# Kernel tuning notes

Hardware: AMD Instinct MI355X
Metric: run time of the kernel (lower is better)

## Reference

```python
import jax, jax.numpy as jnp
import numpy as np

B, S, IN_DIM, HID, H, CS = 4, 4096, 1024, 1024, 16, 16
HD = HID // H
LN_EPS = 1e-5


def setup_inputs() -> dict:
    key = jax.random.key(0)
    ks = jax.random.split(key, 6)
    x = jax.random.normal(ks[0], (B, S, IN_DIM), jnp.float32)
    W_in = jax.random.normal(ks[1], (HID, IN_DIM), jnp.float32) * (IN_DIM ** -0.5)
    ln_g = jnp.ones((HID,), jnp.float32)
    ln_b = jnp.zeros((HID,), jnp.float32)
    W_gate = jax.random.normal(ks[2], (2 * H, HID), jnp.float32) * (HID ** -0.5)
    b_gate = jnp.zeros((2 * H,), jnp.float32)
    raw = 0.5 * float(np.log(1.9 / 0.1))  # atanh(0.9), as in _init_eigenvalues
    eig_raw = jnp.full((H,), raw, jnp.float32) + 0.01 * jax.random.normal(ks[3], (H,), jnp.float32)
    W_out = jax.random.normal(ks[4], (HID, HID), jnp.float32) * (HID ** -0.5)
    return {"x": x, "W_in": W_in, "ln_g": ln_g, "ln_b": ln_b,
            "W_gate": W_gate, "b_gate": b_gate, "eig_raw": eig_raw, "W_out": W_out}


def _chunk_scan(a, b):
    # a: (B,S,H) decay, b: (B,S,H,HD) input; h_t = a_t*h_{t-1} + b_t, h0 = 0
    Bsz, Sl = a.shape[0], a.shape[1]
    N = Sl // CS  # seq_len chosen divisible by chunk_size (pad_len == 0)
    ac = a.reshape(Bsz, N, CS, H)
    bc = b.reshape(Bsz, N, CS, H, HD)
    cum = jnp.cumprod(ac, axis=2)  # (B,N,C,H)
    ones = jnp.ones((Bsz, N, 1, H), a.dtype)
    cum_pad = jnp.concatenate([ones, cum[:, :, :-1]], axis=2)  # shifted cumprod
    # M[i,j] = cum_i / cum_pad_j for i>j, 1 on diag, 0 above
    Mi = cum[:, :, :, None, :]        # (B,N,C,1,H)
    Mj = cum_pad[:, :, None, :, :]    # (B,N,1,C,H)
    M = jnp.where(jnp.abs(Mj) > 1e-8, Mi / Mj, jnp.zeros_like(Mi))
    tril = jnp.tril(jnp.ones((CS, CS), a.dtype))[None, None, :, :, None]
    eye = jnp.eye(CS, dtype=a.dtype)[None, None, :, :, None]
    M = M * tril
    M = M * (1 - eye) + eye  # force exact 1 on diagonal
    # within-chunk contribution: (B,N,C,H,HD)
    h_contrib = jnp.einsum('bnijh,bnjhd->bnihd', M, bc)
    # inter-chunk sequential carry
    cum_T = jnp.moveaxis(cum, 1, 0)            # (N,B,C,H)
    hc_T = jnp.moveaxis(h_contrib, 1, 0)       # (N,B,C,H,HD)

    def step(h, inp):
        cum_n, hc_n = inp
        h_chunk = cum_n[..., None] * h[:, None] + hc_n  # (B,C,H,HD)
        return h_chunk[:, -1], h_chunk

    h0 = jnp.zeros((Bsz, H, HD), a.dtype)
    _, h_all = jax.lax.scan(step, h0, (cum_T, hc_T))   # (N,B,C,H,HD)
    h_all = jnp.moveaxis(h_all, 0, 1).reshape(Bsz, Sl, HID)
    return h_all


def reference(x, W_in, ln_g, ln_b, W_gate, b_gate, eig_raw, W_out):
    Bsz, Sl, _ = x.shape
    xp = x @ W_in.T                               # (B,S,HID)
    mu = jnp.mean(xp, axis=-1, keepdims=True)
    var = jnp.mean((xp - mu) ** 2, axis=-1, keepdims=True)
    xp = (xp - mu) * jax.lax.rsqrt(var + LN_EPS) * ln_g + ln_b
    gates = xp @ W_gate.T + b_gate                # (B,S,2H)
    alpha = jax.nn.sigmoid(gates[..., :H])
    beta = jax.nn.sigmoid(gates[..., H:])
    eig = jnp.tanh(eig_raw)                       # (H,)
    a = eig[None, None, :] * alpha                # (B,S,H)
    x_heads = xp.reshape(Bsz, Sl, H, HD)
    b = beta[..., None] * x_heads                 # (B,S,H,HD)
    h_all = _chunk_scan(a, b)                     # (B,S,HID)
    output = h_all @ W_out.T                      # dropout is identity in eval
    h_final = h_all[:, -1, :]
    return output, h_final
```

## Files before the change

### kernel.cpp

```cpp
#include <hip/hip_runtime.h>
#include <hip/hip_bf16.h>
#include <stdint.h>

#define BATCH 4
#define SEQ   4096
#define HID   1024
#define NH    16
#define HD    64
#define CS    16
#define NCH   256
#define MROWS 16384

typedef __attribute__((ext_vector_type(8))) __bf16 bf16x8;
typedef __attribute__((ext_vector_type(4))) float  f32x4;

__device__ __forceinline__ unsigned short f2bf(float f) {
    union { float f; unsigned u; } x; x.f = f;
    unsigned r = x.u + 0x7FFFu + ((x.u >> 16) & 1u);
    return (unsigned short)(r >> 16);
}
__device__ __forceinline__ float bf2f(unsigned short v) {
    union { unsigned u; float f; } x; x.u = ((unsigned)v) << 16;
    return x.f;
}

__device__ __forceinline__ void async_copy16(void* lds, const void* g) {
    __builtin_amdgcn_global_load_lds(
        (const __attribute__((address_space(1))) unsigned int*)g,
        (__attribute__((address_space(3))) unsigned int*)lds,
        16, 0, 0);
}

#define FENCE() asm volatile("" ::: "memory")
#define BARRIER() do { FENCE(); __builtin_amdgcn_s_barrier(); FENCE(); } while (0)

__global__ __launch_bounds__(256) void convert_all_kernel(
    const float* __restrict__ x, const float* __restrict__ W_in,
    const float* __restrict__ W_out, const float* __restrict__ W_gate,
    unsigned short* __restrict__ xb, unsigned short* __restrict__ Wib,
    unsigned short* __restrict__ Wob, unsigned short* __restrict__ Wgb)
{
    int i = blockIdx.x * 256 + threadIdx.x;
    const float4* src; ushort4* dst; int j;
    if (i < 4194304)      { src = (const float4*)x;      dst = (ushort4*)xb;  j = i; }
    else if (i < 4456448) { src = (const float4*)W_in;   dst = (ushort4*)Wib; j = i - 4194304; }
    else if (i < 4718592) { src = (const float4*)W_out;  dst = (ushort4*)Wob; j = i - 4456448; }
    else if (i < 4726784) { src = (const float4*)W_gate; dst = (ushort4*)Wgb; j = i - 4718592; }
    else return;
    float4 v = src[j];
    ushort4 o;
    o.x = f2bf(v.x); o.y = f2bf(v.y); o.z = f2bf(v.z); o.w = f2bf(v.w);
    dst[j] = o;
}

#define GBM 256
#define GBN 256
#define GBK 64

__global__ __launch_bounds__(512, 2) void gemm256_kernel(
    const unsigned short* __restrict__ A,
    const unsigned short* __restrict__ Bm,
    float* __restrict__ C, int M, int N, int K)
{
    __shared__ unsigned short As[2][GBM][GBK];
    __shared__ unsigned short Bs[2][GBN][GBK];

    const int t = threadIdx.x;
    const int lane = t & 63, w = t >> 6;
    const int wm = w >> 2, wn = w & 3;

    const int nwg = gridDim.x;
    const int cpx = nwg >> 3;
    const int bid = blockIdx.x;
    const int swz = (bid & 7) * cpx + (bid >> 3);
    const int ntile = N >> 8;
    const size_t bm = (size_t)(swz / ntile) * GBM;
    const size_t bn = (size_t)(swz % ntile) * GBN;

    const int srow = t >> 3;
    const int sp   = t & 7;
    const int sgc  = sp ^ (srow & 7);
    const unsigned short* Ag = A  + (bm + srow) * (size_t)K + sgc * 8;
    const unsigned short* Bg = Bm + (bn + srow) * (size_t)K + sgc * 8;

    const int fr = lane & 15, fq = lane >> 4;
    const int frl = fr & 7;

    f32x4 acc[8][4];
#pragma unroll
    for (int x = 0; x < 8; x++)
#pragma unroll
        for (int y = 0; y < 4; y++)
            acc[x][y] = (f32x4){0.f, 0.f, 0.f, 0.f};

    bf16x8 afr[4][2];
    bf16x8 bf0[2][2];
    bf16x8 bf1[2][2];

    auto stage = [&](int par, int h, int k0) {
        if (h < 2) {
            const unsigned short* g = Ag + ((size_t)h * 128) * K + k0;
            unsigned short* l = &As[par][h * 128 + srow][sp * 8];
            async_copy16(l,            g);
            async_copy16(l + 64 * GBK, g + (size_t)64 * K);
        } else {
            const int hh = h - 2;
            const unsigned short* g = Bg + ((size_t)hh * 128) * K + k0;
            unsigned short* l = &Bs[par][hh * 128 + srow][sp * 8];
            async_copy16(l,            g);
            async_copy16(l + 64 * GBK, g + (size_t)64 * K);
        }
    };
    auto rdA = [&](int par, int xh) {
#pragma unroll
        for (int x = 0; x < 4; x++)
#pragma unroll
            for (int kk = 0; kk < 2; kk++)
                afr[x][kk] = *(const bf16x8*)&As[par][wm * 128 + xh * 64 + x * 16 + fr]
                                                    [((kk * 4 + fq) ^ frl) * 8];
    };
    auto rdB = [&](int par, int yh, bf16x8 (&bfv)[2][2]) {
#pragma unroll
        for (int y = 0; y < 2; y++)
#pragma unroll
            for (int kk = 0; kk < 2; kk++)
                bfv[y][kk] = *(const bf16x8*)&Bs[par][wn * 64 + yh * 32 + y * 16 + fr]
                                                    [((kk * 4 + fq) ^ frl) * 8];
    };
    auto mm = [&](bf16x8 (&bfv)[2][2], int x0, int y0) {
        __builtin_amdgcn_s_setprio(1);
#pragma unroll
        for (int kk = 0; kk < 2; kk++)
#pragma unroll
            for (int x = 0; x < 4; x++)
#pragma unroll
                for (int y = 0; y < 2; y++)
                    acc[x0 + x][y0 + y] = __builtin_amdgcn_mfma_f32_16x16x32_bf16(
                        afr[x][kk], bfv[y][kk], acc[x0 + x][y0 + y], 0, 0, 0);
        __builtin_amdgcn_s_setprio(0);
    };

    const int NT = K >> 6;

#pragma unroll
    for (int h = 0; h < 4; h++) stage(0, h, 0);
    asm volatile("s_waitcnt vmcnt(0)" ::: "memory");
    BARRIER();

    int par = 0;
    for (int tt = 0; tt < NT - 1; ++tt, par ^= 1) {
        const int k1 = (tt + 1) << 6;
        stage(par ^ 1, 0, k1);
        asm volatile("s_waitcnt vmcnt(2)" ::: "memory");
        BARRIER();
        rdA(par, 0); rdB(par, 0, bf0);
        mm(bf0, 0, 0);
        BARRIER();
        rdB(par, 1, bf1);
        stage(par ^ 1, 1, k1);
        BARRIER();
        mm(bf1, 0, 2);
        BARRIER();
        rdA(par, 1);
        stage(par ^ 1, 2, k1);
        BARRIER();
        mm(bf0, 4, 0);
        BARRIER();
        stage(par ^ 1, 3, k1);
        BARRIER();
        mm(bf1, 4, 2);
        BARRIER();
    }

    asm volatile("s_waitcnt vmcnt(0)" ::: "memory");
    BARRIER();
    rdA(par, 0); rdB(par, 0, bf0);
    mm(bf0, 0, 0);
    rdB(par, 1, bf1);
    mm(bf1, 0, 2);
    rdA(par, 1);
    mm(bf0, 4, 0);
    mm(bf1, 4, 2);

#pragma unroll
    for (int x = 0; x < 8; x++) {
#pragma unroll
        for (int y = 0; y < 4; y++) {
            const size_t r0 = bm + wm * 128 + x * 16 + fq * 4;
            const size_t c  = bn + wn * 64 + y * 16 + fr;
#pragma unroll
            for (int rg = 0; rg < 4; rg++)
                C[(r0 + rg) * (size_t)N + c] = acc[x][y][rg];
        }
    }
}

__global__ __launch_bounds__(256) void mid_kernel(
    const float* __restrict__ xp,
    const float* __restrict__ ln_g, const float* __restrict__ ln_b,
    const unsigned short* __restrict__ Wgb,
    const float* __restrict__ bg, const float* __restrict__ eig_raw,
    unsigned short* __restrict__ xln,
    float* __restrict__ beta_buf,
    float* __restrict__ cum_out,
    float* __restrict__ c15c,
    float* __restrict__ hc15)
{
    __shared__ unsigned short sx[16][1032];
    __shared__ float red[4][2][64][4];
    __shared__ float sg[16][32];
    __shared__ float scum[16][16];
    const int t = threadIdx.x, lane = t & 63, w = t >> 6;
    const int bn = blockIdx.x;
    const size_t m0 = (size_t)(bn >> 8) * SEQ + (size_t)(bn & 255) * 16;

    const int r = t >> 4, u = t & 15;
    {
        const float* row = xp + (m0 + r) * 1024;
        float4 v[16];
        float s = 0.f, s2 = 0.f;
#pragma unroll
        for (int i = 0; i < 16; i++) {
            v[i] = *(const float4*)(row + u * 4 + i * 64);
            s  += v[i].x + v[i].y + v[i].z + v[i].w;
            s2 += v[i].x * v[i].x + v[i].y * v[i].y + v[i].z * v[i].z + v[i].w * v[i].w;
        }
#pragma unroll
        for (int off = 1; off < 16; off <<= 1) {
            s  += __shfl_xor(s, off, 64);
            s2 += __shfl_xor(s2, off, 64);
        }
        const float mu = s * (1.f / 1024.f);
        const float var = s2 * (1.f / 1024.f) - mu * mu;
        const float sc = rsqrtf(var + 1e-5f);
        unsigned short* orow = xln + (m0 + r) * 1024;
#pragma unroll
        for (int i = 0; i < 16; i++) {
            const int k = u * 4 + i * 64;
            float4 g4 = *(const float4*)(ln_g + k);
            float4 b4 = *(const float4*)(ln_b + k);
            ushort4 o;
            o.x = f2bf((v[i].x - mu) * sc * g4.x + b4.x);
            o.y = f2bf((v[i].y - mu) * sc * g4.y + b4.y);
            o.z = f2bf((v[i].z - mu) * sc * g4.z + b4.z);
            o.w = f2bf((v[i].w - mu) * sc * g4.w + b4.w);
            *(ushort4*)&sx[r][k] = o;
            *(ushort4*)(orow + k) = o;
        }
    }
    __syncthreads();

    const int fr = lane & 15, fq = lane >> 4;
    {
        f32x4 acc0 = (f32x4){0.f,0.f,0.f,0.f}, acc1 = (f32x4){0.f,0.f,0.f,0.f};
        const unsigned short* Wr0 = Wgb + (size_t)fr * 1024;
        const unsigned short* Wr1 = Wgb + (size_t)(16 + fr) * 1024;
#pragma unroll
        for (int ks = 0; ks < 8; ks++) {
            const int k0 = w * 256 + ks * 32 + fq * 8;
            bf16x8 af = *(const bf16x8*)&sx[fr][k0];
            bf16x8 b0 = *(const bf16x8*)(Wr0 + k0);
            bf16x8 b1 = *(const bf16x8*)(Wr1 + k0);
            acc0 = __builtin_amdgcn_mfma_f32_16x16x32_bf16(af, b0, acc0, 0, 0, 0);
            acc1 = __builtin_amdgcn_mfma_f32_16x16x32_bf16(af, b1, acc1, 0, 0, 0);
        }
        *(f32x4*)&red[w][0][lane][0] = acc0;
        *(f32x4*)&red[w][1][lane][0] = acc1;
    }
    __syncthreads();
    if (t < 128) {
        const int y = t >> 6, l = t & 63;
        f32x4 s = *(const f32x4*)&red[0][y][l][0];
#pragma unroll
        for (int ww = 1; ww < 4; ww++) {
            f32x4 p = *(const f32x4*)&red[ww][y][l][0];
            s[0] += p[0]; s[1] += p[1]; s[2] += p[2]; s[3] += p[3];
        }
        const int col = y * 16 + (l & 15);
        const int row0 = (l >> 4) * 4;
        const float bias = bg[col];
#pragma unroll
        for (int rg = 0; rg < 4; rg++)
            sg[row0 + rg][col] = 1.f / (1.f + expf(-(s[rg] + bias)));
    }
    __syncthreads();

    if (t < 16) {
        const float ev = tanhf(eig_raw[t]);
        float c = 1.f;
#pragma unroll
        for (int i = 0; i < 16; i++) { c *= ev * sg[i][t]; scum[i][t] = c; }
    }
    beta_buf[(m0 + r) * 16 + u] = sg[r][16 + u];
    __syncthreads();

    cum_out[(size_t)bn * 256 + t] = scum[t >> 4][t & 15];
    if (t < 16) c15c[bn * 16 + t] = scum[15][t];

    {
        const int h = t >> 4, d0 = (t & 15) * 4;
        float s0 = 0.f, s1 = 0.f, s2 = 0.f, s3 = 0.f;
        float b0 = 0.f, b1 = 0.f, b2 = 0.f, b3 = 0.f;
        float cprev = 1.f;
#pragma unroll
        for (int j = 0; j < 16; j++) {
            const float bt = sg[j][16 + h];
            ushort4 xv = *(const ushort4*)&sx[j][h * 64 + d0];
            b0 = bt * bf2f(xv.x); b1 = bt * bf2f(xv.y);
            b2 = bt * bf2f(xv.z); b3 = bt * bf2f(xv.w);
            if (j < 15) {
                const float inv = (fabsf(cprev) > 1e-8f) ? (1.f / cprev) : 0.f;
                s0 += b0 * inv; s1 += b1 * inv; s2 += b2 * inv; s3 += b3 * inv;
                cprev = scum[j][h];
            }
        }
        const float c15 = scum[15][h];
        float4 o = { c15 * s0 + b0, c15 * s1 + b1, c15 * s2 + b2, c15 * s3 + b3 };
        *(float4*)(hc15 + (size_t)bn * 1024 + h * 64 + d0) = o;
    }
}

__global__ __launch_bounds__(64) void scan2_kernel(
    const float* __restrict__ c15c,
    const float* __restrict__ hc15,
    float* __restrict__ carry_in,
    float* __restrict__ h_final)
{
    const int p = blockIdx.x * 64 + threadIdx.x;
    const int b = p >> 10, hd = p & 1023, h = hd >> 6;
    float carry = 0.f;
#pragma unroll 8
    for (int n = 0; n < NCH; n++) {
        const size_t bn = (size_t)b * NCH + n;
        const float c15 = c15c[bn * 16 + h];
        carry_in[bn * 1024 + hd] = carry;
        carry = c15 * carry + hc15[bn * 1024 + hd];
    }
    h_final[(size_t)b * 1024 + hd] = carry;
}

__global__ __launch_bounds__(256) void scan3_kernel(
    const float* __restrict__ cum_buf,
    const float* __restrict__ beta_buf,
    const unsigned short* __restrict__ xln,
    const float* __restrict__ carry_in,
    unsigned short* __restrict__ hall)
{
    __shared__ float scum[16][16];
    __shared__ float sbeta[16][16];
    const int t = threadIdx.x;
    const int bn = blockIdx.x;
    const size_t m0 = (size_t)(bn >> 8) * SEQ + (size_t)(bn & 255) * 16;

    scum[t >> 4][t & 15]  = cum_buf[(size_t)bn * 256 + t];
    sbeta[t >> 4][t & 15] = beta_buf[(m0 + (t >> 4)) * 16 + (t & 15)];
    __syncthreads();

    const int h = t >> 4, dq = t & 15;
    const size_t off = h * 64 + dq * 4;
    float4 s = *(const float4*)(carry_in + (size_t)bn * 1024 + off);
    float cprev = 1.f;
#pragma unroll
    for (int i = 0; i < 16; i++) {
        ushort4 xv = *(const ushort4*)(xln + (m0 + i) * 1024 + off);
        const float bt = sbeta[i][h];
        const float b0 = bt * bf2f(xv.x), b1 = bt * bf2f(xv.y),
                    b2 = bt * bf2f(xv.z), b3 = bt * bf2f(xv.w);
        const float ci = scum[i][h];
        ushort4 o;
        o.x = f2bf(ci * s.x + b0); o.y = f2bf(ci * s.y + b1);
        o.z = f2bf(ci * s.z + b2); o.w = f2bf(ci * s.w + b3);
        *(ushort4*)(hall + (m0 + i) * 1024 + off) = o;
        const float inv = (fabsf(cprev) > 1e-8f) ? (1.f / cprev) : 0.f;
        s.x += b0 * inv; s.y += b1 * inv; s.z += b2 * inv; s.w += b3 * inv;
        cprev = ci;
    }
}

extern "C" void kernel_launch(void* const* d_in, const int* in_sizes, int n_in,
                              void* d_out, int out_size, void* d_ws, size_t ws_size,
                              hipStream_t stream)
{
    const float* x       = (const float*)d_in[0];
    const float* W_in    = (const float*)d_in[1];
    const float* ln_g    = (const float*)d_in[2];
    const float* ln_b    = (const float*)d_in[3];
    const float* W_gate  = (const float*)d_in[4];
    const float* b_gate  = (const float*)d_in[5];
    const float* eig_raw = (const float*)d_in[6];
    const float* W_out   = (const float*)d_in[7];
    float* out = (float*)d_out;

    char* ws = (char*)d_ws;
    unsigned short* xb   = (unsigned short*)(ws);
    unsigned short* xln  = (unsigned short*)(ws);
    unsigned short* hall = (unsigned short*)(ws + 33554432);
    unsigned short* Wib  = (unsigned short*)(ws + 67108864);
    unsigned short* Wob  = (unsigned short*)(ws + 69206016);
    unsigned short* Wgb  = (unsigned short*)(ws + 71303168);
    float* beta_buf = (float*)(ws + 71368704);
    float* cum_buf  = (float*)(ws + 72417280);
    float* c15c     = (float*)(ws + 73465856);
    float* hc15     = (float*)(ws + 73531392);
    float* carry_in = (float*)(ws + 77725696);

    float* xp = out;
    float* h_final = out + 16777216;

    convert_all_kernel<<<18464, 256, 0, stream>>>(x, W_in, W_out, W_gate, xb, Wib, Wob, Wgb);

    gemm256_kernel<<<256, 512, 0, stream>>>(xb, Wib, xp, MROWS, HID, HID);

    mid_kernel<<<1024, 256, 0, stream>>>(xp, ln_g, ln_b, Wgb, b_gate, eig_raw,
                                         xln, beta_buf, cum_buf, c15c, hc15);

    scan2_kernel<<<64, 64, 0, stream>>>(c15c, hc15, carry_in, h_final);
    scan3_kernel<<<1024, 256, 0, stream>>>(cum_buf, beta_buf, xln, carry_in, hall);

    gemm256_kernel<<<256, 512, 0, stream>>>(hall, Wob, out, MROWS, HID, HID);
}
```

Measured before the change: 264.4 us.

## Restructure GEMM main loop into deeper unrolled prefetch pipeline with finer waitcnts

```diff
diff --git a/kernel.cpp b/kernel.cpp
--- a/kernel.cpp
+++ b/kernel.cpp
@@ -33,6 +33,9 @@
 
 #define FENCE() asm volatile("" ::: "memory")
 #define BARRIER() do { FENCE(); __builtin_amdgcn_s_barrier(); FENCE(); } while (0)
+#define LGKM0_SB() do { asm volatile("s_waitcnt lgkmcnt(0)" ::: "memory"); \
+                        __builtin_amdgcn_sched_barrier(0); } while (0)
+#define VM6() asm volatile("s_waitcnt vmcnt(6)" ::: "memory")
 
 __global__ __launch_bounds__(256) void convert_all_kernel(
     const float* __restrict__ x, const float* __restrict__ W_in,
@@ -94,19 +97,17 @@
             acc[x][y] = (f32x4){0.f, 0.f, 0.f, 0.f};
 
     bf16x8 afr[4][2];
-    bf16x8 bf0[2][2];
-    bf16x8 bf1[2][2];
-
-    auto stage = [&](int par, int h, int k0) {
+    bf16x8 bfr[4][2];
+
+    auto stage = [&](int par, int h, int kt) {
         if (h < 2) {
-            const unsigned short* g = Ag + ((size_t)h * 128) * K + k0;
+            const unsigned short* g = Ag + (size_t)(h * 128) * K + kt;
             unsigned short* l = &As[par][h * 128 + srow][sp * 8];
             async_copy16(l,            g);
             async_copy16(l + 64 * GBK, g + (size_t)64 * K);
         } else {
-            const int hh = h - 2;
-            const unsigned short* g = Bg + ((size_t)hh * 128) * K + k0;
-            unsigned short* l = &Bs[par][hh * 128 + srow][sp * 8];
+            const unsigned short* g = Bg + (size_t)((h - 2) * 128) * K + kt;
+            unsigned short* l = &Bs[par][(h - 2) * 128 + srow][sp * 8];
             async_copy16(l,            g);
             async_copy16(l + 64 * GBK, g + (size_t)64 * K);
         }
@@ -119,68 +120,78 @@
                 afr[x][kk] = *(const bf16x8*)&As[par][wm * 128 + xh * 64 + x * 16 + fr]
                                                     [((kk * 4 + fq) ^ frl) * 8];
     };
-    auto rdB = [&](int par, int yh, bf16x8 (&bfv)[2][2]) {
-#pragma unroll
-        for (int y = 0; y < 2; y++)
+    auto rdB = [&](int par) {
+#pragma unroll
+        for (int y = 0; y < 4; y++)
 #pragma unroll
             for (int kk = 0; kk < 2; kk++)
-                bfv[y][kk] = *(const bf16x8*)&Bs[par][wn * 64 + yh * 32 + y * 16 + fr]
+                bfr[y][kk] = *(const bf16x8*)&Bs[par][wn * 64 + y * 16 + fr]
                                                     [((kk * 4 + fq) ^ frl) * 8];
     };
-    auto mm = [&](bf16x8 (&bfv)[2][2], int x0, int y0) {
+    auto mm = [&](int xh, int yh) {
         __builtin_amdgcn_s_setprio(1);
 #pragma unroll
         for (int kk = 0; kk < 2; kk++)
 #pragma unroll
             for (int x = 0; x < 4; x++)
 #pragma unroll
-                for (int y = 0; y < 2; y++)
-                    acc[x0 + x][y0 + y] = __builtin_amdgcn_mfma_f32_16x16x32_bf16(
-                        afr[x][kk], bfv[y][kk], acc[x0 + x][y0 + y], 0, 0, 0);
+                for (int yy = 0; yy < 2; yy++)
+                    acc[xh * 4 + x][yh * 2 + yy] = __builtin_amdgcn_mfma_f32_16x16x32_bf16(
+                        afr[x][kk], bfr[yh * 2 + yy][kk], acc[xh * 4 + x][yh * 2 + yy], 0, 0, 0);
         __builtin_amdgcn_s_setprio(0);
     };
 
     const int NT = K >> 6;
-
-#pragma unroll
-    for (int h = 0; h < 4; h++) stage(0, h, 0);
-    asm volatile("s_waitcnt vmcnt(0)" ::: "memory");
+    const int kmax = (NT - 1) << 6;
+    auto kt = [&](int tile) { int k = tile << 6; return k > kmax ? kmax : k; };
+
+    stage(0, 2, 0); stage(0, 3, 0); stage(0, 0, 0); stage(0, 1, 0);
+    stage(1, 2, kt(1)); stage(1, 3, kt(1)); stage(1, 0, kt(1));
+    VM6();
     BARRIER();
 
-    int par = 0;
-    for (int tt = 0; tt < NT - 1; ++tt, par ^= 1) {
-        const int k1 = (tt + 1) << 6;
-        stage(par ^ 1, 0, k1);
-        asm volatile("s_waitcnt vmcnt(2)" ::: "memory");
-        BARRIER();
-        rdA(par, 0); rdB(par, 0, bf0);
-        mm(bf0, 0, 0);
-        BARRIER();
-        rdB(par, 1, bf1);
-        stage(par ^ 1, 1, k1);
-        BARRIER();
-        mm(bf1, 0, 2);
-        BARRIER();
-        rdA(par, 1);
-        stage(par ^ 1, 2, k1);
-        BARRIER();
-        mm(bf0, 4, 0);
-        BARRIER();
-        stage(par ^ 1, 3, k1);
-        BARRIER();
-        mm(bf1, 4, 2);
-        BARRIER();
-    }
-
-    asm volatile("s_waitcnt vmcnt(0)" ::: "memory");
-    BARRIER();
-    rdA(par, 0); rdB(par, 0, bf0);
-    mm(bf0, 0, 0);
-    rdB(par, 1, bf1);
-    mm(bf1, 0, 2);
-    rdA(par, 1);
-    mm(bf0, 4, 0);
-    mm(bf1, 4, 2);
+    for (int it = 0; it < (NT >> 1); ++it) {
+        const int T = it << 1;
+        const int kT1 = kt(T + 1), kT2 = kt(T + 2), kT3 = kt(T + 3);
+        rdA(0, 0); rdB(0);
+        stage(1, 1, kT1);
+        BARRIER(); LGKM0_SB();
+        mm(0, 0);
+        BARRIER();
+        stage(0, 2, kT2);
+        BARRIER();
+        mm(0, 1);
+        BARRIER();
+        rdA(0, 1);
+        stage(0, 3, kT2);
+        BARRIER(); LGKM0_SB();
+        mm(1, 0);
+        BARRIER();
+        stage(0, 0, kT2);
+        VM6();
+        BARRIER();
+        mm(1, 1);
+        BARRIER();
+        rdA(1, 0); rdB(1);
+        stage(0, 1, kT2);
+        BARRIER(); LGKM0_SB();
+        mm(0, 0);
+        BARRIER();
+        stage(1, 2, kT3);
+        BARRIER();
+        mm(0, 1);
+        BARRIER();
+        rdA(1, 1);
+        stage(1, 3, kT3);
+        BARRIER(); LGKM0_SB();
+        mm(1, 0);
+        BARRIER();
+        stage(1, 0, kT3);
+        VM6();
+        BARRIER();
+        mm(1, 1);
+        BARRIER();
+    }
 
 #pragma unroll
     for (int x = 0; x < 8; x++) {
@@ -193,6 +204,7 @@
                 C[(r0 + rg) * (size_t)N + c] = acc[x][y][rg];
         }
     }
+    asm volatile("s_waitcnt vmcnt(0)" ::: "memory");
 }
 
 __global__ __launch_bounds__(256) void mid_kernel(
```

After: 264.8 us. About the same (+0.2%).
